# Kernel tuning notes

Measured on AMD Instinct MI355X. Metric: run time of the kernel, lower is better.

Reference implementation:

```python
import jax, jax.numpy as jnp
import numpy as np

B_SZ, SEQ, D_MODEL = 2, 512, 1024
EXPAND, HEAD_DIM = 2, 64
D_INNER = EXPAND * D_MODEL            # 2048
N_HEADS = D_INNER // HEAD_DIM         # 32
D_STATE = 64
EPS = 1e-6
PROJ_DIM = 2 * D_INNER + 2 * N_HEADS * D_STATE + N_HEADS  # 8224


def setup_inputs() -> dict:
    key = jax.random.key(0)
    k = jax.random.split(key, 5)
    return {
        "hidden": jax.random.normal(k[0], (B_SZ, SEQ, D_MODEL), jnp.float32),
        "W_in": 0.02 * jax.random.normal(k[1], (D_MODEL, PROJ_DIM), jnp.float32),
        "dt_bias": 0.5 * jax.random.normal(k[2], (N_HEADS,), jnp.float32),
        "A_log": 0.5 * jax.random.normal(k[3], (N_HEADS,), jnp.float32),
        "norm_weight": jnp.ones((D_INNER,), jnp.float32),
        "W_out": 0.02 * jax.random.normal(k[4], (D_INNER, D_MODEL), jnp.float32),
    }


def _rope(x, theta):
    # x: [b,l,h,n] interleaved pairs (view_as_complex convention); theta: [b,l,h,n//2]
    x0, x1 = x[..., 0::2], x[..., 1::2]
    c, s = jnp.cos(theta), jnp.sin(theta)
    y = jnp.stack([x0 * c - x1 * s, x0 * s + x1 * c], axis=-1)
    return y.reshape(x.shape)


def reference(hidden, W_in, dt_bias, A_log, norm_weight, W_out):
    b, l, _ = hidden.shape
    proj = hidden @ W_in  # [b,l,PROJ_DIM]
    hn = N_HEADS * D_STATE
    z = proj[..., :D_INNER]
    xr = proj[..., D_INNER:2 * D_INNER].reshape(b, l, N_HEADS, HEAD_DIM)
    Bm = proj[..., 2 * D_INNER:2 * D_INNER + hn].reshape(b, l, N_HEADS, D_STATE)
    Cm = proj[..., 2 * D_INNER + hn:2 * D_INNER + 2 * hn].reshape(b, l, N_HEADS, D_STATE)
    dt = jax.nn.softplus(proj[..., -N_HEADS:] + dt_bias)  # [b,l,h]

    A = -jnp.exp(A_log)                 # [h], negative decay
    alpha = jnp.exp(dt * A)             # decay factor
    beta = 0.5 * dt * alpha             # trapezoidal: half-step on previous input
    gamma = 0.5 * dt                    # trapezoidal: half-step on current input

    # data-dependent RoPE: phase is cumulative dt scaled by per-dim inverse freq
    half = D_STATE // 2
    inv_freq = 1.0 / (10000.0 ** (jnp.arange(half, dtype=jnp.float32) / half))
    theta = jnp.cumsum(dt, axis=1)[..., None] * inv_freq  # [b,l,h,half]
    Bm = _rope(Bm, theta)
    Cm = _rope(Cm, theta)

    # shifted (t-1) inputs, zero at t=0 (h starts at 0 so alpha-at-t0 is a no-op)
    Bp = jnp.pad(Bm[:, :-1], ((0, 0), (1, 0), (0, 0), (0, 0)))
    xp = jnp.pad(xr[:, :-1], ((0, 0), (1, 0), (0, 0), (0, 0)))

    tl = lambda t: jnp.moveaxis(t, 1, 0)  # time-major for scan
    xs = (tl(xr), tl(Bm), tl(Cm), tl(Bp), tl(xp), tl(alpha), tl(beta), tl(gamma))
    h0 = jnp.zeros((b, N_HEADS, D_STATE, HEAD_DIM), hidden.dtype)

    def step(h, inp):
        x_t, B_t, C_t, Bprev, xprev, a, bt, g = inp
        h = (a[..., None, None] * h
             + bt[..., None, None] * jnp.einsum('bhn,bhp->bhnp', Bprev, xprev)
             + g[..., None, None] * jnp.einsum('bhn,bhp->bhnp', B_t, x_t))
        y = jnp.einsum('bhn,bhnp->bhp', C_t, h)
        return h, y

    _, ys = jax.lax.scan(step, h0, xs)          # ys: [l,b,h,p]
    y = jnp.moveaxis(ys, 0, 1).reshape(b, l, D_INNER)

    y = y * jax.nn.silu(z)                      # gated output
    rms = jnp.sqrt(jnp.mean(y * y, axis=-1, keepdims=True) + EPS)
    y = y / rms * norm_weight                   # RMSNorm
    return y @ W_out
```

## Files before the change

### kernel.cpp

```cpp
#include <hip/hip_runtime.h>
#include <stdint.h>

typedef __attribute__((ext_vector_type(8))) short short8;
typedef __attribute__((ext_vector_type(8))) unsigned short ushort8;
typedef __attribute__((ext_vector_type(4))) unsigned short usv4;
typedef __attribute__((ext_vector_type(4))) float float4v;

#define B_SZ 2
#define SEQ 512
#define D_MODEL 1024
#define D_INNER 2048
#define N_HEADS 32
#define HEAD_DIM 64
#define D_STATE 64
#define PROJ_DIM 8224
#define NPAD 8320
#define MROWS 1024

__device__ __forceinline__ unsigned short f2bf(float f) {
    unsigned u = __builtin_bit_cast(unsigned, f);
    u += 0x7fffu + ((u >> 16) & 1u);
    return (unsigned short)(u >> 16);
}
__device__ __forceinline__ float bf2f(unsigned short h) {
    return __builtin_bit_cast(float, (unsigned)h << 16);
}

__device__ __forceinline__ void gld16(unsigned short* lds, const unsigned short* g) {
#if __has_builtin(__builtin_amdgcn_global_load_lds)
    __builtin_amdgcn_global_load_lds(
        (const __attribute__((address_space(1))) void*)g,
        (__attribute__((address_space(3))) void*)lds, 16, 0, 0);
#else
    *(short8*)lds = *(const short8*)g;
#endif
}

__device__ void transpose_body(const float* __restrict__ src,
                               unsigned short* __restrict__ dst,
                               int R, int C, int bx, int by, float* T, int tid) {
    int c0 = bx * 64, r0 = by * 64;
    int row = tid >> 2, cg = (tid & 3) * 16;
    #pragma unroll
    for (int k = 0; k < 4; k++) {
        int col = cg + k * 4;
        float4v v;
        if (c0 + col + 3 < C) {
            v = *(const float4v*)&src[(size_t)(r0 + row) * C + c0 + col];
        } else {
            #pragma unroll
            for (int e = 0; e < 4; e++)
                v[e] = (c0 + col + e < C) ? src[(size_t)(r0 + row) * C + c0 + col + e] : 0.f;
        }
        *(float4v*)&T[row * 68 + col] = v;
    }
    __syncthreads();
    int drow = tid >> 2, sg = (tid & 3) * 16;
    ushort8 v[2];
    #pragma unroll
    for (int k = 0; k < 16; k++) v[k >> 3][k & 7] = f2bf(T[(sg + k) * 68 + drow]);
    unsigned short* d = &dst[(size_t)(c0 + drow) * R + r0 + sg];
    *(ushort8*)&d[0] = v[0];
    *(ushort8*)&d[8] = v[1];
}

__global__ __launch_bounds__(256) void prep_fat(
    const float* __restrict__ hidden, const float* __restrict__ W_in,
    const float* __restrict__ W_out, unsigned short* __restrict__ Hb,
    unsigned short* __restrict__ Wt1, unsigned short* __restrict__ Wt2) {
    __shared__ float T[64 * 68];
    int blk = blockIdx.x, tid = threadIdx.x;
    if (blk < 1024) {
        int i = blk * 1024 + tid * 4;
        float4v v = *(const float4v*)&hidden[i];
        usv4 o;
        #pragma unroll
        for (int k = 0; k < 4; k++) o[k] = f2bf(v[k]);
        *(usv4*)&Hb[i] = o;
    } else if (blk < 3104) {
        int q = blk - 1024;
        transpose_body(W_in, Wt1, D_MODEL, PROJ_DIM, q % 130, q / 130, T, tid);
    } else {
        int q = blk - 3104;
        transpose_body(W_out, Wt2, D_INNER, D_MODEL, q % 16, q / 16, T, tid);
    }
}

template <bool BF16OUT>
__global__ __launch_bounds__(256) void gemm_bt(
    const unsigned short* __restrict__ A, const unsigned short* __restrict__ Bt,
    void* __restrict__ Cout, int M, int N, int K, int klen) {
    __shared__ unsigned short As[8192];
    __shared__ unsigned short Bs[8192];
    int tid = threadIdx.x;
    int lane = tid & 63, w = tid >> 6, quad = lane >> 4, l15 = lane & 15;
    int m0 = blockIdx.y * 128, n0 = blockIdx.x * 128;
    int kb = blockIdx.z * klen, ke = kb + klen;
    int wm = (w & 1) * 64, wn = (w >> 1) * 64;
    float4v acc[4][4];
    #pragma unroll
    for (int i = 0; i < 4; i++)
        #pragma unroll
        for (int j = 0; j < 4; j++) acc[i][j] = (float4v){0.f, 0.f, 0.f, 0.f};

    int rs = tid >> 3;
    int gl = ((tid & 7) ^ (rs & 7)) * 8;
    const unsigned short* ap = &A [(size_t)(m0 + rs) * K + gl];
    const unsigned short* bp = &Bt[(size_t)(n0 + rs) * K + gl];
    int rx = l15 & 7;

    for (int k0 = kb; k0 < ke; k0 += 64) {
        __syncthreads();
        #pragma unroll
        for (int p = 0; p < 4; p++) {
            gld16(&As[p * 2048 + tid * 8], ap + (size_t)(p * 32) * K + k0);
            gld16(&Bs[p * 2048 + tid * 8], bp + (size_t)(p * 32) * K + k0);
        }
        __syncthreads();
        #pragma unroll
        for (int kq = 0; kq < 2; kq++) {
            short8 af[4], bfr[4];
            #pragma unroll
            for (int mt = 0; mt < 4; mt++)
                af[mt] = *(const short8*)&As[(wm + mt * 16 + l15) * 64 + (((kq << 2) + quad) ^ rx) * 8];
            #pragma unroll
            for (int nt = 0; nt < 4; nt++)
                bfr[nt] = *(const short8*)&Bs[(wn + nt * 16 + l15) * 64 + (((kq << 2) + quad) ^ rx) * 8];
            #pragma unroll
            for (int mt = 0; mt < 4; mt++)
                #pragma unroll
                for (int nt = 0; nt < 4; nt++)
                    acc[mt][nt] = __builtin_amdgcn_mfma_f32_16x16x32_bf16(
                        af[mt], bfr[nt], acc[mt][nt], 0, 0, 0);
        }
    }
    #pragma unroll
    for (int mt = 0; mt < 4; mt++)
        #pragma unroll
        for (int nt = 0; nt < 4; nt++)
            #pragma unroll
            for (int r = 0; r < 4; r++) {
                int row = m0 + wm + mt * 16 + quad * 4 + r;
                int col = n0 + wn + nt * 16 + l15;
                if (col < N) {
                    if (BF16OUT)
                        ((unsigned short*)Cout)[(size_t)blockIdx.z * M * N + (size_t)row * N + col]
                            = f2bf(acc[mt][nt][r]);
                    else
                        ((float*)Cout)[(size_t)blockIdx.z * M * N + (size_t)row * N + col]
                            = acc[mt][nt][r];
                }
            }
}

__global__ __launch_bounds__(256) void reduce4(
    const float* __restrict__ P, float* __restrict__ out, int n) {
    int i = (blockIdx.x * 256 + threadIdx.x) * 4;
    float4v s = *(const float4v*)&P[i];
    #pragma unroll
    for (int z = 1; z < 4; z++) {
        float4v v = *(const float4v*)&P[(size_t)z * n + i];
        #pragma unroll
        for (int k = 0; k < 4; k++) s[k] += v[k];
    }
    *(float4v*)&out[i] = s;
}

__global__ __launch_bounds__(256) void dt_scan(
    const unsigned short* __restrict__ proj, const float* __restrict__ dt_bias,
    float* __restrict__ dt_arr, float* __restrict__ cum_arr) {
    __shared__ float chs[8];
    int bh = blockIdx.x;
    int b = bh >> 5, h = bh & 31;
    int tid = threadIdx.x, lane = tid & 63, w = tid >> 6;
    float bias = dt_bias[h];
    int t0 = w * 64 + lane, t1 = 256 + w * 64 + lane;
    float raw0 = bf2f(proj[(size_t)(b * SEQ + t0) * PROJ_DIM + 8192 + h]) + bias;
    float raw1 = bf2f(proj[(size_t)(b * SEQ + t1) * PROJ_DIM + 8192 + h]) + bias;
    float dt0 = raw0 > 20.f ? raw0 : log1pf(expf(raw0));
    float dt1 = raw1 > 20.f ? raw1 : log1pf(expf(raw1));
    float v0 = dt0, v1 = dt1;
    #pragma unroll
    for (int d = 1; d < 64; d <<= 1) {
        float n0 = __shfl_up(v0, d, 64);
        float n1 = __shfl_up(v1, d, 64);
        if (lane >= d) { v0 += n0; v1 += n1; }
    }
    if (lane == 63) { chs[w] = v0; chs[4 + w] = v1; }
    __syncthreads();
    float off0 = 0.f, off1 = 0.f;
    #pragma unroll
    for (int c = 0; c < 8; c++) {
        float s = chs[c];
        if (c < w) off0 += s;
        if (c < 4 + w) off1 += s;
    }
    dt_arr[bh * SEQ + t0] = dt0;  cum_arr[bh * SEQ + t0] = off0 + v0;
    dt_arr[bh * SEQ + t1] = dt1;  cum_arr[bh * SEQ + t1] = off1 + v1;
}

__global__ __launch_bounds__(256) void pack_fat(
    const unsigned short* __restrict__ proj, const float* __restrict__ cum_arr,
    unsigned short* __restrict__ Bh, unsigned short* __restrict__ Ch,
    unsigned short* __restrict__ Xt, float* __restrict__ y_ws) {
    __shared__ unsigned short XT[64 * 72];
    int blk = blockIdx.x, tid = threadIdx.x;
    if (blk < 1024) {
        int m = blk, b = m >> 9, t = m & 511;
        const float k_l2 = 13.287712379549449f / 32.f;
        #pragma unroll
        for (int i = 0; i < 4; i++) {
            int q = i * 256 + tid;
            int h = q >> 5, j = q & 31;
            float cum = cum_arr[(b * 32 + h) * SEQ + t];
            float th = cum * exp2f(-(float)j * k_l2);
            float s, c;
            __sincosf(th, &s, &c);
            size_t rb = (size_t)m * PROJ_DIM;
            unsigned bu = *(const unsigned*)&proj[rb + 4096 + h * 64 + 2 * j];
            unsigned cu = *(const unsigned*)&proj[rb + 6144 + h * 64 + 2 * j];
            float b0 = bf2f((unsigned short)(bu & 0xffff)), b1 = bf2f((unsigned short)(bu >> 16));
            float c0 = bf2f((unsigned short)(cu & 0xffff)), c1 = bf2f((unsigned short)(cu >> 16));
            size_t dst = ((size_t)(b * 32 + h) * SEQ + t) * 64 + 2 * j;
            unsigned ob = (unsigned)f2bf(b0 * c - b1 * s) | ((unsigned)f2bf(b0 * s + b1 * c) << 16);
            unsigned oc = (unsigned)f2bf(c0 * c - c1 * s) | ((unsigned)f2bf(c0 * s + c1 * c) << 16);
            *(unsigned*)&Bh[dst] = ob;
            *(unsigned*)&Ch[dst] = oc;
        }
    } else if (blk < 1536) {
        int q = blk - 1024;
        int bh = q >> 3, s0 = (q & 7) * 64;
        int b = bh >> 5, h = bh & 31;
        int r = tid >> 2, cg = (tid & 3) * 16;
        const unsigned short* src = &proj[(size_t)(b * SEQ + s0 + r) * PROJ_DIM + 2048 + h * 64 + cg];
        *(ushort8*)&XT[r * 72 + cg]     = *(const ushort8*)&src[0];
        *(ushort8*)&XT[r * 72 + cg + 8] = *(const ushort8*)&src[8];
        __syncthreads();
        int p = tid >> 2, sg = (tid & 3) * 16;
        ushort8 v[2];
        #pragma unroll
        for (int k = 0; k < 16; k++) v[k >> 3][k & 7] = XT[(sg + k) * 72 + p];
        unsigned short* dst = &Xt[((size_t)bh * 64 + p) * SEQ + s0 + sg];
        *(ushort8*)&dst[0] = v[0];
        *(ushort8*)&dst[8] = v[1];
    } else {
        int q = blk - 1536;
        *(float4v*)&y_ws[(size_t)q * 1024 + tid * 4] = (float4v){0.f, 0.f, 0.f, 0.f};
    }
}

__global__ __launch_bounds__(256) void attn_tile(
    const unsigned short* __restrict__ Bh, const unsigned short* __restrict__ Ch,
    const unsigned short* __restrict__ Xt, const float* __restrict__ dt_arr,
    const float* __restrict__ cum_arr, const float* __restrict__ A_log,
    float* __restrict__ y_ws) {
    __shared__ unsigned short Bs[4096];
    __shared__ unsigned short Xs[4096];
    __shared__ unsigned short Ps[4096];
    int pid = blockIdx.x;
    int qt = 0, base = 0;
    while (base + qt + 1 <= pid) { base += qt + 1; qt++; }
    int st = pid - base;
    int bh = blockIdx.y;
    int b = bh >> 5, h = bh & 31;
    float Aneg = -expf(A_log[h]);
    int tid = threadIdx.x, lane = tid & 63, w = tid >> 6;
    int quad = lane >> 4, l15 = lane & 15;
    int rx = l15 & 7;

    {
        int srow = tid >> 3, sg = tid & 7;
        int srow2 = srow + 32;
        const unsigned short* bsrc = Bh + ((size_t)bh * SEQ + st * 64) * 64;
        gld16(&Bs[tid * 8],         bsrc + srow * 64  + ((sg ^ (srow & 7)) * 8));
        gld16(&Bs[(tid + 256) * 8], bsrc + srow2 * 64 + ((sg ^ (srow2 & 7)) * 8));
        const unsigned short* xsrc = Xt + (size_t)bh * 64 * SEQ + st * 64;
        gld16(&Xs[tid * 8],         xsrc + (size_t)srow * SEQ  + ((sg ^ (srow & 7)) * 8));
        gld16(&Xs[(tid + 256) * 8], xsrc + (size_t)srow2 * SEQ + ((sg ^ (srow2 & 7)) * 8));
    }

    int qrow = qt * 64 + w * 16 + l15;
    const unsigned short* Cptr = Ch + ((size_t)bh * SEQ + qrow) * 64;
    short8 cf[2];
    cf[0] = *(const short8*)&Cptr[quad * 8];
    cf[1] = *(const short8*)&Cptr[32 + quad * 8];

    int trow[4];
    float cumt[4];
    #pragma unroll
    for (int r = 0; r < 4; r++) {
        trow[r] = qt * 64 + w * 16 + quad * 4 + r;
        cumt[r] = cum_arr[bh * SEQ + trow[r]];
    }

    __syncthreads();

    float4v sacc[4];
    #pragma unroll
    for (int i = 0; i < 4; i++) sacc[i] = (float4v){0.f, 0.f, 0.f, 0.f};
    #pragma unroll
    for (int kk = 0; kk < 2; kk++)
        #pragma unroll
        for (int nt = 0; nt < 4; nt++) {
            short8 bf8 = *(const short8*)&Bs[(nt * 16 + l15) * 64 + (((kk << 2) + quad) ^ rx) * 8];
            sacc[nt] = __builtin_amdgcn_mfma_f32_16x16x32_bf16(cf[kk], bf8, sacc[nt], 0, 0, 0);
        }
    #pragma unroll
    for (int nt = 0; nt < 4; nt++) {
        int s = st * 64 + nt * 16 + l15;
        float cums = cum_arr[bh * SEQ + s];
        float dts = dt_arr[bh * SEQ + s];
        float dts1 = (s + 1 < SEQ) ? dt_arr[bh * SEQ + s + 1] : 0.f;
        #pragma unroll
        for (int r = 0; r < 4; r++) {
            int t = trow[r];
            float wgt = (s > t) ? 0.f
                      : expf(Aneg * (cumt[r] - cums)) * 0.5f * (dts + ((s < t) ? dts1 : 0.f));
            int row = quad * 4 + r;
            int col = nt * 16 + l15;
            Ps[w * 1024 + row * 64 + (((col >> 3) ^ (row & 7)) << 3) + (col & 7)]
                = f2bf(sacc[nt][r] * wgt);
        }
    }
    float4v yacc[4];
    #pragma unroll
    for (int i = 0; i < 4; i++) yacc[i] = (float4v){0.f, 0.f, 0.f, 0.f};
    #pragma unroll
    for (int kk = 0; kk < 2; kk++) {
        short8 af = *(const short8*)&Ps[w * 1024 + l15 * 64 + (((kk << 2) + quad) ^ rx) * 8];
        #pragma unroll
        for (int pt = 0; pt < 4; pt++) {
            short8 xf = *(const short8*)&Xs[(pt * 16 + l15) * 64 + (((kk << 2) + quad) ^ rx) * 8];
            yacc[pt] = __builtin_amdgcn_mfma_f32_16x16x32_bf16(af, xf, yacc[pt], 0, 0, 0);
        }
    }
    #pragma unroll
    for (int pt = 0; pt < 4; pt++)
        #pragma unroll
        for (int r = 0; r < 4; r++) {
            int t = trow[r];
            int p = pt * 16 + l15;
            unsafeAtomicAdd(&y_ws[((size_t)b * SEQ + t) * D_INNER + h * 64 + p], yacc[pt][r]);
        }
}

__global__ __launch_bounds__(256) void gated_rmsnorm(
    const float* __restrict__ y_ws, const unsigned short* __restrict__ proj,
    const float* __restrict__ nw, unsigned short* __restrict__ Y2) {
    __shared__ float red[4];
    int m = blockIdx.x, tid = threadIdx.x;
    const float* yrow = y_ws + (size_t)m * D_INNER;
    const unsigned short* zrow = proj + (size_t)m * PROJ_DIM;
    int j0 = tid * 8;
    ushort8 zv = *(const ushort8*)&zrow[j0];
    float v[8];
    float ss = 0.f;
    #pragma unroll
    for (int k = 0; k < 8; k++) {
        float y = yrow[j0 + k];
        float z = bf2f(zv[k]);
        float g = y * (z / (1.f + expf(-z)));
        v[k] = g;
        ss += g * g;
    }
    #pragma unroll
    for (int d = 32; d > 0; d >>= 1) ss += __shfl_down(ss, d, 64);
    if ((tid & 63) == 0) red[tid >> 6] = ss;
    __syncthreads();
    float tot = red[0] + red[1] + red[2] + red[3];
    float inv = 1.0f / sqrtf(tot / (float)D_INNER + 1e-6f);
    #pragma unroll
    for (int k = 0; k < 8; k++)
        Y2[(size_t)m * D_INNER + j0 + k] = f2bf(v[k] * inv * nw[j0 + k]);
}


extern "C" void kernel_launch(void* const* d_in, const int* in_sizes, int n_in,
                              void* d_out, int out_size, void* d_ws, size_t ws_size,
                              hipStream_t stream) {
    const float* hidden   = (const float*)d_in[0];
    const float* W_in     = (const float*)d_in[1];
    const float* dt_bias  = (const float*)d_in[2];
    const float* A_log    = (const float*)d_in[3];
    const float* norm_w   = (const float*)d_in[4];
    const float* W_out    = (const float*)d_in[5];
    float* out = (float*)d_out;

    char* ws = (char*)d_ws;
    unsigned short* Wt1  = (unsigned short*)(ws);
    unsigned short* Hb   = (unsigned short*)(ws + 17039360);
    unsigned short* proj = (unsigned short*)(ws + 19136512);
    float* dt_arr        = (float*)(ws + 35979264);
    float* cum_arr       = (float*)(ws + 36110336);
    unsigned short* Bh   = (unsigned short*)(ws + 36241408);
    unsigned short* Ch   = (unsigned short*)(ws + 40435712);
    unsigned short* Xt   = (unsigned short*)(ws + 44630016);
    float* y_ws          = (float*)(ws + 48824320);
    unsigned short* Y2   = (unsigned short*)(ws + 57212928);
    unsigned short* Wt2  = (unsigned short*)(ws + 61407232);
    float* Pk = (float*)proj;

    prep_fat<<<3616, 256, 0, stream>>>(hidden, W_in, W_out, Hb, Wt1, Wt2);
    gemm_bt<true><<<dim3(NPAD / 128, MROWS / 128, 1), 256, 0, stream>>>(
        Hb, Wt1, proj, MROWS, PROJ_DIM, D_MODEL, D_MODEL);
    dt_scan<<<64, 256, 0, stream>>>(proj, dt_bias, dt_arr, cum_arr);
    pack_fat<<<3584, 256, 0, stream>>>(proj, cum_arr, Bh, Ch, Xt, y_ws);
    attn_tile<<<dim3(36, 64), 256, 0, stream>>>(Bh, Ch, Xt, dt_arr, cum_arr, A_log, y_ws);
    gated_rmsnorm<<<MROWS, 256, 0, stream>>>(y_ws, proj, norm_w, Y2);
    gemm_bt<false><<<dim3(D_MODEL / 128, MROWS / 128, 4), 256, 0, stream>>>(
        Y2, Wt2, Pk, MROWS, D_MODEL, D_INNER, D_INNER / 4);
    reduce4<<<MROWS * D_MODEL / 1024, 256, 0, stream>>>(Pk, out, MROWS * D_MODEL);
}
```

Baseline: 198.5 us.

## Replace split-K reduce kernel with atomics and pair source tiles in attention

The output GEMM now splits K eight ways and accumulates straight into the zeroed output with float atomics. This removes the separate reduce4 kernel and its partial-sum buffer traffic, and the output is zeroed inside pack_fat. The attention tile kernel now has each block handle up to two source tiles for a query tile, accumulating y in registers. That halves the number of global atomic adds into y_ws and cuts the block count from 36 to 20 per head. The cost is more atomic contention on the output, a non-deterministic summation order, and more serial work per attention block.

```diff
diff --git a/kernel.cpp b/kernel.cpp
--- a/kernel.cpp
+++ b/kernel.cpp
@@ -86,7 +86,7 @@
     }
 }
 
-template <bool BF16OUT>
+template <int MODE>
 __global__ __launch_bounds__(256) void gemm_bt(
     const unsigned short* __restrict__ A, const unsigned short* __restrict__ Bt,
     void* __restrict__ Cout, int M, int N, int K, int klen) {
@@ -143,27 +143,12 @@
                 int row = m0 + wm + mt * 16 + quad * 4 + r;
                 int col = n0 + wn + nt * 16 + l15;
                 if (col < N) {
-                    if (BF16OUT)
-                        ((unsigned short*)Cout)[(size_t)blockIdx.z * M * N + (size_t)row * N + col]
-                            = f2bf(acc[mt][nt][r]);
+                    if (MODE == 1)
+                        ((unsigned short*)Cout)[(size_t)row * N + col] = f2bf(acc[mt][nt][r]);
                     else
-                        ((float*)Cout)[(size_t)blockIdx.z * M * N + (size_t)row * N + col]
-                            = acc[mt][nt][r];
+                        unsafeAtomicAdd(&((float*)Cout)[(size_t)row * N + col], acc[mt][nt][r]);
                 }
             }
-}
-
-__global__ __launch_bounds__(256) void reduce4(
-    const float* __restrict__ P, float* __restrict__ out, int n) {
-    int i = (blockIdx.x * 256 + threadIdx.x) * 4;
-    float4v s = *(const float4v*)&P[i];
-    #pragma unroll
-    for (int z = 1; z < 4; z++) {
-        float4v v = *(const float4v*)&P[(size_t)z * n + i];
-        #pragma unroll
-        for (int k = 0; k < 4; k++) s[k] += v[k];
-    }
-    *(float4v*)&out[i] = s;
 }
 
 __global__ __launch_bounds__(256) void dt_scan(
@@ -202,7 +187,8 @@
 __global__ __launch_bounds__(256) void pack_fat(
     const unsigned short* __restrict__ proj, const float* __restrict__ cum_arr,
     unsigned short* __restrict__ Bh, unsigned short* __restrict__ Ch,
-    unsigned short* __restrict__ Xt, float* __restrict__ y_ws) {
+    unsigned short* __restrict__ Xt, float* __restrict__ y_ws,
+    float* __restrict__ outz) {
     __shared__ unsigned short XT[64 * 72];
     int blk = blockIdx.x, tid = threadIdx.x;
     if (blk < 1024) {
@@ -243,9 +229,12 @@
         unsigned short* dst = &Xt[((size_t)bh * 64 + p) * SEQ + s0 + sg];
         *(ushort8*)&dst[0] = v[0];
         *(ushort8*)&dst[8] = v[1];
-    } else {
+    } else if (blk < 3584) {
         int q = blk - 1536;
         *(float4v*)&y_ws[(size_t)q * 1024 + tid * 4] = (float4v){0.f, 0.f, 0.f, 0.f};
+    } else {
+        int q = blk - 3584;
+        *(float4v*)&outz[(size_t)q * 1024 + tid * 4] = (float4v){0.f, 0.f, 0.f, 0.f};
     }
 }
 
@@ -258,9 +247,10 @@
     __shared__ unsigned short Xs[4096];
     __shared__ unsigned short Ps[4096];
     int pid = blockIdx.x;
-    int qt = 0, base = 0;
-    while (base + qt + 1 <= pid) { base += qt + 1; qt++; }
-    int st = pid - base;
+    int qt = 0;
+    while (pid >= ((qt + 2) >> 1)) { pid -= ((qt + 2) >> 1); qt++; }
+    int st0 = pid * 2;
+    int nst = (st0 + 1 <= qt) ? 2 : 1;
     int bh = blockIdx.y;
     int b = bh >> 5, h = bh & 31;
     float Aneg = -expf(A_log[h]);
@@ -268,17 +258,6 @@
     int quad = lane >> 4, l15 = lane & 15;
     int rx = l15 & 7;
 
-    {
-        int srow = tid >> 3, sg = tid & 7;
-        int srow2 = srow + 32;
-        const unsigned short* bsrc = Bh + ((size_t)bh * SEQ + st * 64) * 64;
-        gld16(&Bs[tid * 8],         bsrc + srow * 64  + ((sg ^ (srow & 7)) * 8));
-        gld16(&Bs[(tid + 256) * 8], bsrc + srow2 * 64 + ((sg ^ (srow2 & 7)) * 8));
-        const unsigned short* xsrc = Xt + (size_t)bh * 64 * SEQ + st * 64;
-        gld16(&Xs[tid * 8],         xsrc + (size_t)srow * SEQ  + ((sg ^ (srow & 7)) * 8));
-        gld16(&Xs[(tid + 256) * 8], xsrc + (size_t)srow2 * SEQ + ((sg ^ (srow2 & 7)) * 8));
-    }
-
     int qrow = qt * 64 + w * 16 + l15;
     const unsigned short* Cptr = Ch + ((size_t)bh * SEQ + qrow) * 64;
     short8 cf[2];
@@ -292,46 +271,59 @@
         trow[r] = qt * 64 + w * 16 + quad * 4 + r;
         cumt[r] = cum_arr[bh * SEQ + trow[r]];
     }
-
-    __syncthreads();
-
-    float4v sacc[4];
-    #pragma unroll
-    for (int i = 0; i < 4; i++) sacc[i] = (float4v){0.f, 0.f, 0.f, 0.f};
-    #pragma unroll
-    for (int kk = 0; kk < 2; kk++)
+    float4v yacc[4];
+    #pragma unroll
+    for (int i = 0; i < 4; i++) yacc[i] = (float4v){0.f, 0.f, 0.f, 0.f};
+
+    int srow = tid >> 3, sg = tid & 7;
+    int swz = (sg ^ (srow & 7)) * 8;
+
+    for (int si = 0; si < nst; si++) {
+        int st = st0 + si;
+        __syncthreads();
+        const unsigned short* bsrc = Bh + ((size_t)bh * SEQ + st * 64) * 64;
+        gld16(&Bs[tid * 8],         bsrc + srow * 64 + swz);
+        gld16(&Bs[(tid + 256) * 8], bsrc + (srow + 32) * 64 + swz);
+        const unsigned short* xsrc = Xt + (size_t)bh * 64 * SEQ + st * 64;
+        gld16(&Xs[tid * 8],         xsrc + (size_t)srow * SEQ + swz);
+        gld16(&Xs[(tid + 256) * 8], xsrc + (size_t)(srow + 32) * SEQ + swz);
+        __syncthreads();
+
+        float4v sacc[4];
+        #pragma unroll
+        for (int i = 0; i < 4; i++) sacc[i] = (float4v){0.f, 0.f, 0.f, 0.f};
+        #pragma unroll
+        for (int kk = 0; kk < 2; kk++)
+            #pragma unroll
+            for (int nt = 0; nt < 4; nt++) {
+                short8 bf8 = *(const short8*)&Bs[(nt * 16 + l15) * 64 + (((kk << 2) + quad) ^ rx) * 8];
+                sacc[nt] = __builtin_amdgcn_mfma_f32_16x16x32_bf16(cf[kk], bf8, sacc[nt], 0, 0, 0);
+            }
         #pragma unroll
         for (int nt = 0; nt < 4; nt++) {
-            short8 bf8 = *(const short8*)&Bs[(nt * 16 + l15) * 64 + (((kk << 2) + quad) ^ rx) * 8];
-            sacc[nt] = __builtin_amdgcn_mfma_f32_16x16x32_bf16(cf[kk], bf8, sacc[nt], 0, 0, 0);
-        }
-    #pragma unroll
-    for (int nt = 0; nt < 4; nt++) {
-        int s = st * 64 + nt * 16 + l15;
-        float cums = cum_arr[bh * SEQ + s];
-        float dts = dt_arr[bh * SEQ + s];
-        float dts1 = (s + 1 < SEQ) ? dt_arr[bh * SEQ + s + 1] : 0.f;
-        #pragma unroll
-        for (int r = 0; r < 4; r++) {
-            int t = trow[r];
-            float wgt = (s > t) ? 0.f
-                      : expf(Aneg * (cumt[r] - cums)) * 0.5f * (dts + ((s < t) ? dts1 : 0.f));
-            int row = quad * 4 + r;
-            int col = nt * 16 + l15;
-            Ps[w * 1024 + row * 64 + (((col >> 3) ^ (row & 7)) << 3) + (col & 7)]
-                = f2bf(sacc[nt][r] * wgt);
-        }
-    }
-    float4v yacc[4];
-    #pragma unroll
-    for (int i = 0; i < 4; i++) yacc[i] = (float4v){0.f, 0.f, 0.f, 0.f};
-    #pragma unroll
-    for (int kk = 0; kk < 2; kk++) {
-        short8 af = *(const short8*)&Ps[w * 1024 + l15 * 64 + (((kk << 2) + quad) ^ rx) * 8];
-        #pragma unroll
-        for (int pt = 0; pt < 4; pt++) {
-            short8 xf = *(const short8*)&Xs[(pt * 16 + l15) * 64 + (((kk << 2) + quad) ^ rx) * 8];
-            yacc[pt] = __builtin_amdgcn_mfma_f32_16x16x32_bf16(af, xf, yacc[pt], 0, 0, 0);
+            int s = st * 64 + nt * 16 + l15;
+            float cums = cum_arr[bh * SEQ + s];
+            float dts = dt_arr[bh * SEQ + s];
+            float dts1 = (s + 1 < SEQ) ? dt_arr[bh * SEQ + s + 1] : 0.f;
+            #pragma unroll
+            for (int r = 0; r < 4; r++) {
+                int t = trow[r];
+                float wgt = (s > t) ? 0.f
+                          : expf(Aneg * (cumt[r] - cums)) * 0.5f * (dts + ((s < t) ? dts1 : 0.f));
+                int row = quad * 4 + r;
+                int col = nt * 16 + l15;
+                Ps[w * 1024 + row * 64 + (((col >> 3) ^ (row & 7)) << 3) + (col & 7)]
+                    = f2bf(sacc[nt][r] * wgt);
+            }
+        }
+        #pragma unroll
+        for (int kk = 0; kk < 2; kk++) {
+            short8 af = *(const short8*)&Ps[w * 1024 + l15 * 64 + (((kk << 2) + quad) ^ rx) * 8];
+            #pragma unroll
+            for (int pt = 0; pt < 4; pt++) {
+                short8 xf = *(const short8*)&Xs[(pt * 16 + l15) * 64 + (((kk << 2) + quad) ^ rx) * 8];
+                yacc[pt] = __builtin_amdgcn_mfma_f32_16x16x32_bf16(af, xf, yacc[pt], 0, 0, 0);
+            }
         }
     }
     #pragma unroll
@@ -398,16 +390,14 @@
     float* y_ws          = (float*)(ws + 48824320);
     unsigned short* Y2   = (unsigned short*)(ws + 57212928);
     unsigned short* Wt2  = (unsigned short*)(ws + 61407232);
-    float* Pk = (float*)proj;
 
     prep_fat<<<3616, 256, 0, stream>>>(hidden, W_in, W_out, Hb, Wt1, Wt2);
-    gemm_bt<true><<<dim3(NPAD / 128, MROWS / 128, 1), 256, 0, stream>>>(
+    gemm_bt<1><<<dim3(NPAD / 128, MROWS / 128, 1), 256, 0, stream>>>(
         Hb, Wt1, proj, MROWS, PROJ_DIM, D_MODEL, D_MODEL);
     dt_scan<<<64, 256, 0, stream>>>(proj, dt_bias, dt_arr, cum_arr);
-    pack_fat<<<3584, 256, 0, stream>>>(proj, cum_arr, Bh, Ch, Xt, y_ws);
-    attn_tile<<<dim3(36, 64), 256, 0, stream>>>(Bh, Ch, Xt, dt_arr, cum_arr, A_log, y_ws);
+    pack_fat<<<4608, 256, 0, stream>>>(proj, cum_arr, Bh, Ch, Xt, y_ws, out);
+    attn_tile<<<dim3(20, 64), 256, 0, stream>>>(Bh, Ch, Xt, dt_arr, cum_arr, A_log, y_ws);
     gated_rmsnorm<<<MROWS, 256, 0, stream>>>(y_ws, proj, norm_w, Y2);
-    gemm_bt<false><<<dim3(D_MODEL / 128, MROWS / 128, 4), 256, 0, stream>>>(
-        Y2, Wt2, Pk, MROWS, D_MODEL, D_INNER, D_INNER / 4);
-    reduce4<<<MROWS * D_MODEL / 1024, 256, 0, stream>>>(Pk, out, MROWS * D_MODEL);
-}
+    gemm_bt<2><<<dim3(D_MODEL / 128, MROWS / 128, 8), 256, 0, stream>>>(
+        Y2, Wt2, out, MROWS, D_MODEL, D_INNER, D_INNER / 8);
+}
```

Result: no change. 199.3 us (+0.4%).

## Replace atomic accumulation in attn_tile with per-slot partial buffers

Applied to the files above, without the earlier changes.

Each attn_tile block now processes up to two source tiles for one query tile, accumulating locally, and writes plain stores to a per-slot partial buffer instead of issuing float atomics into a zeroed workspace. gated_rmsnorm sums the variable number of partials per row, and the zeroing blocks in pack_fat are removed. This removes atomic contention and the memset pass, at the cost of extra partial-buffer memory traffic and fewer, longer attn blocks.

```diff
diff --git a/kernel.cpp b/kernel.cpp
--- a/kernel.cpp
+++ b/kernel.cpp
@@ -144,8 +144,7 @@
                 int col = n0 + wn + nt * 16 + l15;
                 if (col < N) {
                     if (BF16OUT)
-                        ((unsigned short*)Cout)[(size_t)blockIdx.z * M * N + (size_t)row * N + col]
-                            = f2bf(acc[mt][nt][r]);
+                        ((unsigned short*)Cout)[(size_t)row * N + col] = f2bf(acc[mt][nt][r]);
                     else
                         ((float*)Cout)[(size_t)blockIdx.z * M * N + (size_t)row * N + col]
                             = acc[mt][nt][r];
@@ -202,7 +201,7 @@
 __global__ __launch_bounds__(256) void pack_fat(
     const unsigned short* __restrict__ proj, const float* __restrict__ cum_arr,
     unsigned short* __restrict__ Bh, unsigned short* __restrict__ Ch,
-    unsigned short* __restrict__ Xt, float* __restrict__ y_ws) {
+    unsigned short* __restrict__ Xt) {
     __shared__ unsigned short XT[64 * 72];
     int blk = blockIdx.x, tid = threadIdx.x;
     if (blk < 1024) {
@@ -227,7 +226,7 @@
             *(unsigned*)&Bh[dst] = ob;
             *(unsigned*)&Ch[dst] = oc;
         }
-    } else if (blk < 1536) {
+    } else {
         int q = blk - 1024;
         int bh = q >> 3, s0 = (q & 7) * 64;
         int b = bh >> 5, h = bh & 31;
@@ -243,9 +242,6 @@
         unsigned short* dst = &Xt[((size_t)bh * 64 + p) * SEQ + s0 + sg];
         *(ushort8*)&dst[0] = v[0];
         *(ushort8*)&dst[8] = v[1];
-    } else {
-        int q = blk - 1536;
-        *(float4v*)&y_ws[(size_t)q * 1024 + tid * 4] = (float4v){0.f, 0.f, 0.f, 0.f};
     }
 }
 
@@ -253,14 +249,16 @@
     const unsigned short* __restrict__ Bh, const unsigned short* __restrict__ Ch,
     const unsigned short* __restrict__ Xt, const float* __restrict__ dt_arr,
     const float* __restrict__ cum_arr, const float* __restrict__ A_log,
-    float* __restrict__ y_ws) {
+    float* __restrict__ y_part) {
     __shared__ unsigned short Bs[4096];
     __shared__ unsigned short Xs[4096];
     __shared__ unsigned short Ps[4096];
     int pid = blockIdx.x;
-    int qt = 0, base = 0;
-    while (base + qt + 1 <= pid) { base += qt + 1; qt++; }
-    int st = pid - base;
+    int qt = 0;
+    while (pid >= ((qt + 2) >> 1)) { pid -= ((qt + 2) >> 1); qt++; }
+    int slot = pid;
+    int st0 = pid * 2;
+    int nst = (st0 + 1 <= qt) ? 2 : 1;
     int bh = blockIdx.y;
     int b = bh >> 5, h = bh & 31;
     float Aneg = -expf(A_log[h]);
@@ -268,17 +266,6 @@
     int quad = lane >> 4, l15 = lane & 15;
     int rx = l15 & 7;
 
-    {
-        int srow = tid >> 3, sg = tid & 7;
-        int srow2 = srow + 32;
-        const unsigned short* bsrc = Bh + ((size_t)bh * SEQ + st * 64) * 64;
-        gld16(&Bs[tid * 8],         bsrc + srow * 64  + ((sg ^ (srow & 7)) * 8));
-        gld16(&Bs[(tid + 256) * 8], bsrc + srow2 * 64 + ((sg ^ (srow2 & 7)) * 8));
-        const unsigned short* xsrc = Xt + (size_t)bh * 64 * SEQ + st * 64;
-        gld16(&Xs[tid * 8],         xsrc + (size_t)srow * SEQ  + ((sg ^ (srow & 7)) * 8));
-        gld16(&Xs[(tid + 256) * 8], xsrc + (size_t)srow2 * SEQ + ((sg ^ (srow2 & 7)) * 8));
-    }
-
     int qrow = qt * 64 + w * 16 + l15;
     const unsigned short* Cptr = Ch + ((size_t)bh * SEQ + qrow) * 64;
     short8 cf[2];
@@ -292,72 +279,97 @@
         trow[r] = qt * 64 + w * 16 + quad * 4 + r;
         cumt[r] = cum_arr[bh * SEQ + trow[r]];
     }
-
-    __syncthreads();
-
-    float4v sacc[4];
-    #pragma unroll
-    for (int i = 0; i < 4; i++) sacc[i] = (float4v){0.f, 0.f, 0.f, 0.f};
-    #pragma unroll
-    for (int kk = 0; kk < 2; kk++)
+    float4v yacc[4];
+    #pragma unroll
+    for (int i = 0; i < 4; i++) yacc[i] = (float4v){0.f, 0.f, 0.f, 0.f};
+
+    int srow = tid >> 3, sg = tid & 7;
+    int swz = (sg ^ (srow & 7)) * 8;
+
+    for (int si = 0; si < nst; si++) {
+        int st = st0 + si;
+        __syncthreads();
+        const unsigned short* bsrc = Bh + ((size_t)bh * SEQ + st * 64) * 64;
+        gld16(&Bs[tid * 8],         bsrc + srow * 64 + swz);
+        gld16(&Bs[(tid + 256) * 8], bsrc + (srow + 32) * 64 + swz);
+        const unsigned short* xsrc = Xt + (size_t)bh * 64 * SEQ + st * 64;
+        gld16(&Xs[tid * 8],         xsrc + (size_t)srow * SEQ + swz);
+        gld16(&Xs[(tid + 256) * 8], xsrc + (size_t)(srow + 32) * SEQ + swz);
+        __syncthreads();
+
+        float4v sacc[4];
+        #pragma unroll
+        for (int i = 0; i < 4; i++) sacc[i] = (float4v){0.f, 0.f, 0.f, 0.f};
+        #pragma unroll
+        for (int kk = 0; kk < 2; kk++)
+            #pragma unroll
+            for (int nt = 0; nt < 4; nt++) {
+                short8 bf8 = *(const short8*)&Bs[(nt * 16 + l15) * 64 + (((kk << 2) + quad) ^ rx) * 8];
+                sacc[nt] = __builtin_amdgcn_mfma_f32_16x16x32_bf16(cf[kk], bf8, sacc[nt], 0, 0, 0);
+            }
         #pragma unroll
         for (int nt = 0; nt < 4; nt++) {
-            short8 bf8 = *(const short8*)&Bs[(nt * 16 + l15) * 64 + (((kk << 2) + quad) ^ rx) * 8];
-            sacc[nt] = __builtin_amdgcn_mfma_f32_16x16x32_bf16(cf[kk], bf8, sacc[nt], 0, 0, 0);
-        }
-    #pragma unroll
-    for (int nt = 0; nt < 4; nt++) {
-        int s = st * 64 + nt * 16 + l15;
-        float cums = cum_arr[bh * SEQ + s];
-        float dts = dt_arr[bh * SEQ + s];
-        float dts1 = (s + 1 < SEQ) ? dt_arr[bh * SEQ + s + 1] : 0.f;
-        #pragma unroll
-        for (int r = 0; r < 4; r++) {
-            int t = trow[r];
-            float wgt = (s > t) ? 0.f
-                      : expf(Aneg * (cumt[r] - cums)) * 0.5f * (dts + ((s < t) ? dts1 : 0.f));
-            int row = quad * 4 + r;
-            int col = nt * 16 + l15;
-            Ps[w * 1024 + row * 64 + (((col >> 3) ^ (row & 7)) << 3) + (col & 7)]
-                = f2bf(sacc[nt][r] * wgt);
-        }
-    }
-    float4v yacc[4];
-    #pragma unroll
-    for (int i = 0; i < 4; i++) yacc[i] = (float4v){0.f, 0.f, 0.f, 0.f};
-    #pragma unroll
-    for (int kk = 0; kk < 2; kk++) {
-        short8 af = *(const short8*)&Ps[w * 1024 + l15 * 64 + (((kk << 2) + quad) ^ rx) * 8];
-        #pragma unroll
-        for (int pt = 0; pt < 4; pt++) {
-            short8 xf = *(const short8*)&Xs[(pt * 16 + l15) * 64 + (((kk << 2) + quad) ^ rx) * 8];
-            yacc[pt] = __builtin_amdgcn_mfma_f32_16x16x32_bf16(af, xf, yacc[pt], 0, 0, 0);
-        }
-    }
+            int s = st * 64 + nt * 16 + l15;
+            float cums = cum_arr[bh * SEQ + s];
+            float dts = dt_arr[bh * SEQ + s];
+            float dts1 = (s + 1 < SEQ) ? dt_arr[bh * SEQ + s + 1] : 0.f;
+            #pragma unroll
+            for (int r = 0; r < 4; r++) {
+                int t = trow[r];
+                float wgt = (s > t) ? 0.f
+                          : expf(Aneg * (cumt[r] - cums)) * 0.5f * (dts + ((s < t) ? dts1 : 0.f));
+                int row = quad * 4 + r;
+                int col = nt * 16 + l15;
+                Ps[w * 1024 + row * 64 + (((col >> 3) ^ (row & 7)) << 3) + (col & 7)]
+                    = f2bf(sacc[nt][r] * wgt);
+            }
+        }
+        #pragma unroll
+        for (int kk = 0; kk < 2; kk++) {
+            short8 af = *(const short8*)&Ps[w * 1024 + l15 * 64 + (((kk << 2) + quad) ^ rx) * 8];
+            #pragma unroll
+            for (int pt = 0; pt < 4; pt++) {
+                short8 xf = *(const short8*)&Xs[(pt * 16 + l15) * 64 + (((kk << 2) + quad) ^ rx) * 8];
+                yacc[pt] = __builtin_amdgcn_mfma_f32_16x16x32_bf16(af, xf, yacc[pt], 0, 0, 0);
+            }
+        }
+    }
+    float* yp = y_part + (size_t)slot * ((size_t)MROWS * D_INNER);
     #pragma unroll
     for (int pt = 0; pt < 4; pt++)
         #pragma unroll
         for (int r = 0; r < 4; r++) {
             int t = trow[r];
             int p = pt * 16 + l15;
-            unsafeAtomicAdd(&y_ws[((size_t)b * SEQ + t) * D_INNER + h * 64 + p], yacc[pt][r]);
+            yp[((size_t)b * SEQ + t) * D_INNER + h * 64 + p] = yacc[pt][r];
         }
 }
 
 __global__ __launch_bounds__(256) void gated_rmsnorm(
-    const float* __restrict__ y_ws, const unsigned short* __restrict__ proj,
+    const float* __restrict__ y_part, const unsigned short* __restrict__ proj,
     const float* __restrict__ nw, unsigned short* __restrict__ Y2) {
     __shared__ float red[4];
     int m = blockIdx.x, tid = threadIdx.x;
-    const float* yrow = y_ws + (size_t)m * D_INNER;
+    int t = m & 511;
+    int ns = ((t >> 6) + 2) >> 1;
     const unsigned short* zrow = proj + (size_t)m * PROJ_DIM;
     int j0 = tid * 8;
+    float acc8[8];
+    #pragma unroll
+    for (int k = 0; k < 8; k++) acc8[k] = 0.f;
+    for (int p = 0; p < ns; p++) {
+        const float* yr = y_part + (size_t)p * ((size_t)MROWS * D_INNER) + (size_t)m * D_INNER + j0;
+        float4v a = *(const float4v*)&yr[0];
+        float4v c = *(const float4v*)&yr[4];
+        acc8[0] += a[0]; acc8[1] += a[1]; acc8[2] += a[2]; acc8[3] += a[3];
+        acc8[4] += c[0]; acc8[5] += c[1]; acc8[6] += c[2]; acc8[7] += c[3];
+    }
     ushort8 zv = *(const ushort8*)&zrow[j0];
     float v[8];
     float ss = 0.f;
     #pragma unroll
     for (int k = 0; k < 8; k++) {
-        float y = yrow[j0 + k];
+        float y = acc8[k];
         float z = bf2f(zv[k]);
         float g = y * (z / (1.f + expf(-z)));
         v[k] = g;
@@ -395,18 +407,18 @@
     unsigned short* Bh   = (unsigned short*)(ws + 36241408);
     unsigned short* Ch   = (unsigned short*)(ws + 40435712);
     unsigned short* Xt   = (unsigned short*)(ws + 44630016);
-    float* y_ws          = (float*)(ws + 48824320);
     unsigned short* Y2   = (unsigned short*)(ws + 57212928);
     unsigned short* Wt2  = (unsigned short*)(ws + 61407232);
+    float* y_part        = (float*)(ws + 65601536);
     float* Pk = (float*)proj;
 
     prep_fat<<<3616, 256, 0, stream>>>(hidden, W_in, W_out, Hb, Wt1, Wt2);
     gemm_bt<true><<<dim3(NPAD / 128, MROWS / 128, 1), 256, 0, stream>>>(
         Hb, Wt1, proj, MROWS, PROJ_DIM, D_MODEL, D_MODEL);
     dt_scan<<<64, 256, 0, stream>>>(proj, dt_bias, dt_arr, cum_arr);
-    pack_fat<<<3584, 256, 0, stream>>>(proj, cum_arr, Bh, Ch, Xt, y_ws);
-    attn_tile<<<dim3(36, 64), 256, 0, stream>>>(Bh, Ch, Xt, dt_arr, cum_arr, A_log, y_ws);
-    gated_rmsnorm<<<MROWS, 256, 0, stream>>>(y_ws, proj, norm_w, Y2);
+    pack_fat<<<1536, 256, 0, stream>>>(proj, cum_arr, Bh, Ch, Xt);
+    attn_tile<<<dim3(20, 64), 256, 0, stream>>>(Bh, Ch, Xt, dt_arr, cum_arr, A_log, y_part);
+    gated_rmsnorm<<<MROWS, 256, 0, stream>>>(y_part, proj, norm_w, Y2);
     gemm_bt<false><<<dim3(D_MODEL / 128, MROWS / 128, 4), 256, 0, stream>>>(
         Y2, Wt2, Pk, MROWS, D_MODEL, D_INNER, D_INNER / 4);
     reduce4<<<MROWS * D_MODEL / 1024, 256, 0, stream>>>(Pk, out, MROWS * D_MODEL);
```

Result: faster. 183.0 us (-7.8%).
